# Kernel tuning notes

Measured on AMD Instinct MI355X. Metric: run time of the kernel, lower is better.

## Reference

```python
import jax, jax.numpy as jnp
import numpy as np

B, H, W, D = 4, 64, 64, 384
M, P = 12, 9
DH = D // M             # 32 head dim
DFF = 3 * D             # 1152 FFN hidden
N = H * W               # 4096 queries (single level)


def setup_inputs():
    key = jax.random.key(0)
    ks = jax.random.split(key, 12)
    g = lambda k, s, sc=0.02: jax.random.normal(k, s, jnp.float32) * sc
    return {
        "x": jax.random.normal(ks[0], (B, D, H, W), jnp.float32),
        "qry_masks": jnp.zeros((B, H, W), jnp.float32),
        "so_w": g(ks[1], (M * P * 2, D)), "so_b": g(ks[2], (M * P * 2,)),
        "aw_w": g(ks[3], (M * P, D)), "aw_b": g(ks[4], (M * P,)),
        "vp_w": g(ks[5], (D, D)), "vp_b": jnp.zeros((D,), jnp.float32),
        "op_w": g(ks[6], (D, D)), "op_b": jnp.zeros((D,), jnp.float32),
        "ln1_g": jnp.ones((D,), jnp.float32), "ln1_b": jnp.zeros((D,), jnp.float32),
        "w1": g(ks[7], (DFF, D)), "w2": g(ks[8], (D, DFF)),
        "ln2_g": jnp.ones((D,), jnp.float32), "ln2_b": jnp.zeros((D,), jnp.float32),
        "level_embed": g(ks[9], (1, D), 1.0),
    }


def _layernorm(x, g, b, eps=1e-5):
    mu = x.mean(-1, keepdims=True)
    v = ((x - mu) ** 2).mean(-1, keepdims=True)
    return (x - mu) * jax.lax.rsqrt(v + eps) * g + b


def _sine_pos(mask):
    # mask: [B,H,W] bool. mmdet SinePositionalEncoding(num_feats=D//2, normalize=True)
    not_mask = (~mask).astype(jnp.float32)
    y = jnp.cumsum(not_mask, 1)
    x = jnp.cumsum(not_mask, 2)
    eps, scale = 1e-6, 2.0 * np.pi
    y = y / (y[:, -1:, :] + eps) * scale
    x = x / (x[:, :, -1:] + eps) * scale
    nf = D // 2
    dim_t = 10000.0 ** (2.0 * (jnp.arange(nf) // 2).astype(jnp.float32) / nf)
    px, py = x[..., None] / dim_t, y[..., None] / dim_t

    def interleave(p):
        return jnp.stack([jnp.sin(p[..., 0::2]), jnp.cos(p[..., 1::2])], -1).reshape(p.shape[:-1] + (nf,))

    return jnp.concatenate([interleave(py), interleave(px)], -1)  # [B,H,W,D]


def _bilinear_gather(v, px, py):
    # v: [B,M,HW,DH]; px,py: [B,M,NP] pixel coords (grid_sample align_corners=False, zero pad)
    x0 = jnp.floor(px); y0 = jnp.floor(py)
    lx, ly = px - x0, py - y0
    x0i, y0i = x0.astype(jnp.int32), y0.astype(jnp.int32)
    out = jnp.zeros(v.shape[:2] + (px.shape[-1], v.shape[-1]), v.dtype)
    for dx, dy, wgt in ((0, 0, (1 - lx) * (1 - ly)), (1, 0, lx * (1 - ly)),
                        (0, 1, (1 - lx) * ly), (1, 1, lx * ly)):
        xi, yi = x0i + dx, y0i + dy
        valid = ((xi >= 0) & (xi < W) & (yi >= 0) & (yi < H)).astype(v.dtype)
        idx = jnp.clip(yi, 0, H - 1) * W + jnp.clip(xi, 0, W - 1)
        g = jnp.take_along_axis(v, idx[..., None], axis=2)  # [B,M,NP,DH]
        out = out + (wgt * valid)[..., None] * g
    return out


def _msdeform_attn(q, value_in, ref, mask_flat,
                   so_w, so_b, aw_w, aw_b, vp_w, vp_b, op_w, op_b):
    value = value_in @ vp_w.T + vp_b                      # [B,N,D]
    value = jnp.where(mask_flat[..., None], 0.0, value)
    so = (q @ so_w.T + so_b).reshape(B, N, M, P, 2)       # single level
    aw = jax.nn.softmax((q @ aw_w.T + aw_b).reshape(B, N, M, P), axis=-1)
    norm = jnp.array([W, H], jnp.float32)
    loc = ref[:, :, None, None, :] + so / norm            # [B,N,M,P,2] in [0,1]
    v = value.reshape(B, N, M, DH).transpose(0, 2, 1, 3)  # [B,M,HW,DH]
    px = (loc[..., 0] * W - 0.5).transpose(0, 2, 1, 3).reshape(B, M, N * P)
    py = (loc[..., 1] * H - 0.5).transpose(0, 2, 1, 3).reshape(B, M, N * P)
    sampled = _bilinear_gather(v, px, py).reshape(B, M, N, P, DH)
    out = jnp.einsum('bmnpd,bnmp->bnmd', sampled, aw).reshape(B, N, D)
    return out @ op_w.T + op_b


def reference(x, qry_masks, so_w, so_b, aw_w, aw_b, vp_w, vp_b, op_w, op_b,
              ln1_g, ln1_b, w1, w2, ln2_g, ln2_b, level_embed):
    mask = (qry_masks == 255.0)                           # [B,H,W] bool
    pos = _sine_pos(mask).reshape(B, N, D) + level_embed[0]
    src = x.reshape(B, D, N).transpose(0, 2, 1)           # [B,N,D]
    mask_flat = mask.reshape(B, N)
    gy, gx = jnp.meshgrid((jnp.arange(H, dtype=jnp.float32) + 0.5) / H,
                          (jnp.arange(W, dtype=jnp.float32) + 0.5) / W, indexing='ij')
    ref = jnp.stack([gx.reshape(-1), gy.reshape(-1)], -1)[None]  # [1,N,2] (x,y)
    q = src
    attn = _msdeform_attn(q + pos, q, ref, mask_flat,
                          so_w, so_b, aw_w, aw_b, vp_w, vp_b, op_w, op_b)
    q = _layernorm(q + attn, ln1_g, ln1_b)
    q = _layernorm(q + jax.nn.relu(q @ w1.T) @ w2.T, ln2_g, ln2_b)
    return q.transpose(0, 2, 1).reshape(B, D, H, W)
```

## Files before the change

### kernel.cpp

```cpp
#include <hip/hip_runtime.h>
#include <math.h>

#define Bc   4
#define Hc   64
#define Wc   64
#define Dc   384
#define Nc   4096
#define Mc   12
#define Pc   9
#define DHc  32
#define DFFc 1152
#define BNc  (Bc*Nc)

typedef __attribute__((ext_vector_type(8))) short short8;
typedef __attribute__((ext_vector_type(4))) float floatx4;

__device__ __forceinline__ ushort f2bf(float f) {
    union { float f; unsigned u; } v; v.f = f;
    unsigned r = v.u + 0x7fffu + ((v.u >> 16) & 1u);
    return (ushort)(r >> 16);
}
__device__ __forceinline__ float bf2f(ushort u) {
    union { unsigned u; float f; } v; v.u = (unsigned)u << 16; return v.f;
}

__device__ __forceinline__ void gload_lds16(const void* g, void* l) {
    __builtin_amdgcn_global_load_lds(
        (const __attribute__((address_space(1))) void*)(uintptr_t)g,
        (__attribute__((address_space(3))) void*)(uintptr_t)l,
        16, 0, 0);
}

#define SOW_N  82944
#define AWW_N  41472
#define VPW_N  147456
#define OPW_N  147456
#define W1_N   442368
#define W2_N   442368
#define WTOT   1304064

__global__ void init_kernel(const float* __restrict__ so_w,
                            const float* __restrict__ aw_w,
                            const float* __restrict__ vp_w,
                            const float* __restrict__ op_w,
                            const float* __restrict__ w1,
                            const float* __restrict__ w2,
                            const float* __restrict__ so_b,
                            const float* __restrict__ aw_b,
                            const float* __restrict__ qmask,
                            ushort* __restrict__ out,
                            float* __restrict__ bias_out,
                            float* __restrict__ cum_y,
                            float* __restrict__ cum_x) {
    int i = blockIdx.x * 256 + threadIdx.x;
    if (i < WTOT) {
        float v;
        int j = i;
        if (j < SOW_N) v = so_w[j];
        else if ((j -= SOW_N) < AWW_N) v = aw_w[j];
        else if ((j -= AWW_N) < VPW_N) v = vp_w[j];
        else if ((j -= VPW_N) < OPW_N) v = op_w[j];
        else if ((j -= OPW_N) < W1_N)  v = w1[j];
        else { j -= W1_N; v = w2[j]; }
        out[i] = f2bf(v);
        return;
    }
    int j = i - WTOT;
    if (j < 384) {
        bias_out[j] = (j < 216) ? so_b[j] : (j < 324 ? aw_b[j - 216] : 0.f);
        return;
    }
    int t = j - 384;
    if (t < Bc * Wc) {
        int b = t / Wc, w = t % Wc;
        float run = 0.f;
        for (int h = 0; h < Hc; ++h) {
            run += (qmask[(b * Hc + h) * Wc + w] == 255.0f) ? 0.f : 1.f;
            cum_y[(b * Hc + h) * Wc + w] = run;
        }
    } else if (t < Bc * Wc + Bc * Hc) {
        int t2 = t - Bc * Wc;
        int b = t2 / Hc, h = t2 % Hc;
        float run = 0.f;
        for (int w = 0; w < Wc; ++w) {
            run += (qmask[(b * Hc + h) * Wc + w] == 255.0f) ? 0.f : 1.f;
            cum_x[(b * Hc + h) * Wc + w] = run;
        }
    }
}

__global__ void transpose_pos_kernel(const float* __restrict__ x,
                                     const float* __restrict__ cum_y,
                                     const float* __restrict__ cum_x,
                                     const float* __restrict__ level_embed,
                                     ushort* __restrict__ src_bf,
                                     ushort* __restrict__ qpos_bf) {
    __shared__ float tile[32][33];
    int b  = blockIdx.z;
    int n0 = blockIdx.x * 32, d0 = blockIdx.y * 32;
    int tx = threadIdx.x, ty = threadIdx.y;
    tile[ty][tx] = x[((size_t)b * Dc + (d0 + ty)) * Nc + (n0 + tx)];
    __syncthreads();
    int n = n0 + ty, d = d0 + tx;
    float v = tile[tx][ty];
    size_t oi = ((size_t)b * Nc + n) * Dc + d;
    src_bf[oi] = f2bf(v);
    int h = n >> 6, w = n & 63;
    const float TWO_PI = 6.28318530717958647692f;
    float vy = cum_y[(b * Hc + h) * Wc + w] /
               (cum_y[(b * Hc + (Hc - 1)) * Wc + w] + 1e-6f) * TWO_PI;
    float vx = cum_x[(b * Hc + h) * Wc + w] /
               (cum_x[(b * Hc + h) * Wc + (Wc - 1)] + 1e-6f) * TWO_PI;
    int   i  = (d < 192) ? d : d - 192;
    float vv = (d < 192) ? vy : vx;
    float e   = (float)(i >> 1) * (2.0f / 192.0f);
    float idt = exp2f(e * -13.28771237954945f);
    float ang = vv * idt;
    float pe  = (i & 1) ? __cosf(ang) : __sinf(ang);
    qpos_bf[oi] = f2bf(v + pe + level_embed[d]);
}

template <int KT>
__device__ __forceinline__ void gemm_core(
        const ushort* __restrict__ A, const ushort* __restrict__ Wt,
        const float* __restrict__ bias,
        float* __restrict__ Cf, ushort* __restrict__ Cb,
        int Nout, int relu, const float* __restrict__ qmask,
        ushort* As, ushort* Bs) {
    constexpr int NCH = KT / 32;
    const int tid  = threadIdx.x;
    const int m0   = blockIdx.x * 128;
    const int n0   = blockIdx.y * 128;
    const int lane = tid & 63;
    const int wv   = tid >> 6;
    const int wr   = (wv >> 1) * 64;
    const int wc   = (wv & 1) * 64;
    const int quad = lane >> 4;
    const int lrow = lane & 15;
    const int srow = wv * 32 + (lane >> 2);
    const int scol = (lane & 3) * 8;

    floatx4 acc[4][4];
    #pragma unroll
    for (int i = 0; i < 4; ++i)
        #pragma unroll
        for (int j = 0; j < 4; ++j)
            acc[i][j] = (floatx4)(0.f);

    #pragma unroll
    for (int s = 0; s < 2; ++s) {
        gload_lds16(A  + (size_t)(m0 + srow + s * 16) * KT + scol,
                    As + wv * 1024 + s * 512);
        gload_lds16(Wt + (size_t)(n0 + srow + s * 16) * KT + scol,
                    Bs + wv * 1024 + s * 512);
    }

    for (int c = 0; c < NCH; ++c) {
        const int cur = c & 1;
        __syncthreads();
        if (c + 1 < NCH) {
            const int k0 = (c + 1) * 32;
            #pragma unroll
            for (int s = 0; s < 2; ++s) {
                gload_lds16(A  + (size_t)(m0 + srow + s * 16) * KT + k0 + scol,
                            As + (cur ^ 1) * 4096 + wv * 1024 + s * 512);
                gload_lds16(Wt + (size_t)(n0 + srow + s * 16) * KT + k0 + scol,
                            Bs + (cur ^ 1) * 4096 + wv * 1024 + s * 512);
            }
        }
        short8 afr[4], bfr[4];
        #pragma unroll
        for (int i = 0; i < 4; ++i)
            afr[i] = *(const short8*)(As + cur * 4096 +
                                      (wr + i * 16 + lrow) * 32 + quad * 8);
        #pragma unroll
        for (int j = 0; j < 4; ++j)
            bfr[j] = *(const short8*)(Bs + cur * 4096 +
                                      (wc + j * 16 + lrow) * 32 + quad * 8);
        #pragma unroll
        for (int i = 0; i < 4; ++i)
            #pragma unroll
            for (int j = 0; j < 4; ++j)
                acc[i][j] = __builtin_amdgcn_mfma_f32_16x16x32_bf16(
                    afr[i], bfr[j], acc[i][j], 0, 0, 0);
    }

    float mz[4][4];
    #pragma unroll
    for (int i = 0; i < 4; ++i)
        #pragma unroll
        for (int r = 0; r < 4; ++r) {
            int row = m0 + wr + i * 16 + quad * 4 + r;
            mz[i][r] = (qmask && qmask[row] == 255.0f) ? 0.f : 1.f;
        }

    #pragma unroll
    for (int i = 0; i < 4; ++i) {
        #pragma unroll
        for (int j = 0; j < 4; ++j) {
            int col = n0 + wc + j * 16 + lrow;
            if (col >= Nout) continue;
            float bsv = bias ? bias[col] : 0.f;
            #pragma unroll
            for (int r = 0; r < 4; ++r) {
                int row = m0 + wr + i * 16 + quad * 4 + r;
                float v = acc[i][j][r] + bsv;
                if (relu) v = fmaxf(v, 0.f);
                v *= mz[i][r];
                if (Cf) Cf[(size_t)row * Nout + col] = v;
                if (Cb) Cb[(size_t)row * Nout + col] = f2bf(v);
            }
        }
    }
}

template <int KT>
__global__ __launch_bounds__(256) void gemm_single_kernel(
        const ushort* __restrict__ A, const ushort* __restrict__ Wt,
        const float* __restrict__ bias,
        float* __restrict__ Cf, ushort* __restrict__ Cb,
        int Nout, int relu, const float* __restrict__ qmask) {
    __shared__ ushort As[2 * 128 * 32];
    __shared__ ushort Bs[2 * 128 * 32];
    gemm_core<KT>(A, Wt, bias, Cf, Cb, Nout, relu, qmask, As, Bs);
}

__global__ __launch_bounds__(256) void gemm_dual_kernel(
        const ushort* __restrict__ A0, const ushort* __restrict__ W0,
        const float* __restrict__ b0, float* __restrict__ Cf0,
        const ushort* __restrict__ A1, const ushort* __restrict__ W1,
        const float* __restrict__ b1, ushort* __restrict__ Cb1,
        const float* __restrict__ qmask) {
    __shared__ ushort As[2 * 128 * 32];
    __shared__ ushort Bs[2 * 128 * 32];
    if (blockIdx.z == 0)
        gemm_core<384>(A0, W0, b0, Cf0, nullptr, 384, 0, nullptr, As, Bs);
    else
        gemm_core<384>(A1, W1, b1, nullptr, Cb1, 384, 0, qmask, As, Bs);
}

template <int KT, int MODE>
__global__ __launch_bounds__(512) void gemm_fullrow_kernel(
        const ushort* __restrict__ A, const ushort* __restrict__ Wt,
        const float* __restrict__ bias, const void* __restrict__ resid,
        const float* __restrict__ g, const float* __restrict__ beta,
        float* __restrict__ outf, ushort* __restrict__ outb) {
    constexpr int NCH = KT / 32;
    __shared__ ushort smem[28672];
    __shared__ float eps1[8][64], eps2[8][64];
    __shared__ float mu_l[64], rs_l[64];
    ushort* As = smem;
    ushort* Bs = smem + 4096;
    const int tid  = threadIdx.x;
    const int lane = tid & 63;
    const int wv   = tid >> 6;
    const int quad = lane >> 4;
    const int lrow = lane & 15;
    const int m0   = blockIdx.x * 64;
    const int srow = lane >> 2;
    const int scol = (lane & 3) * 8;

    floatx4 acc[4][3];
    #pragma unroll
    for (int i = 0; i < 4; ++i)
        #pragma unroll
        for (int j = 0; j < 3; ++j)
            acc[i][j] = (floatx4)(0.f);

    if (wv < 4)
        gload_lds16(A + (size_t)(m0 + wv * 16 + srow) * KT + scol,
                    As + wv * 512);
    #pragma unroll
    for (int s = 0; s < 3; ++s)
        gload_lds16(Wt + (size_t)(wv * 48 + s * 16 + srow) * KT + scol,
                    Bs + wv * 1536 + s * 512);

    for (int c = 0; c < NCH; ++c) {
        const int cur = c & 1;
        __syncthreads();
        if (c + 1 < NCH) {
            const int k0 = (c + 1) * 32;
            if (wv < 4)
                gload_lds16(A + (size_t)(m0 + wv * 16 + srow) * KT + k0 + scol,
                            As + (cur ^ 1) * 2048 + wv * 512);
            #pragma unroll
            for (int s = 0; s < 3; ++s)
                gload_lds16(Wt + (size_t)(wv * 48 + s * 16 + srow) * KT + k0 + scol,
                            Bs + (cur ^ 1) * 12288 + wv * 1536 + s * 512);
        }
        short8 afr[4], bfr[3];
        #pragma unroll
        for (int i = 0; i < 4; ++i)
            afr[i] = *(const short8*)(As + cur * 2048 +
                                      (i * 16 + lrow) * 32 + quad * 8);
        #pragma unroll
        for (int j = 0; j < 3; ++j)
            bfr[j] = *(const short8*)(Bs + cur * 12288 +
                                      (wv * 48 + j * 16 + lrow) * 32 + quad * 8);
        #pragma unroll
        for (int i = 0; i < 4; ++i)
            #pragma unroll
            for (int j = 0; j < 3; ++j)
                acc[i][j] = __builtin_amdgcn_mfma_f32_16x16x32_bf16(
                    afr[i], bfr[j], acc[i][j], 0, 0, 0);
    }

    float s1[16], s2[16];
    #pragma unroll
    for (int k = 0; k < 16; ++k) { s1[k] = 0.f; s2[k] = 0.f; }
    #pragma unroll
    for (int i = 0; i < 4; ++i) {
        #pragma unroll
        for (int r = 0; r < 4; ++r) {
            int rl = i * 16 + quad * 4 + r;
            #pragma unroll
            for (int j = 0; j < 3; ++j) {
                int col = wv * 48 + j * 16 + lrow;
                float t = acc[i][j][r];
                if (bias) t += bias[col];
                if (MODE == 0)
                    t += bf2f(((const ushort*)resid)[(size_t)(m0 + rl) * Dc + col]);
                else
                    t += ((const float*)resid)[(size_t)(m0 + rl) * Dc + col];
                acc[i][j][r] = t;
                s1[i * 4 + r] += t;
                s2[i * 4 + r] += t * t;
            }
        }
    }
    #pragma unroll
    for (int m = 1; m < 16; m <<= 1) {
        #pragma unroll
        for (int k = 0; k < 16; ++k) {
            s1[k] += __shfl_xor(s1[k], m);
            s2[k] += __shfl_xor(s2[k], m);
        }
    }
    if (lrow == 0) {
        #pragma unroll
        for (int i = 0; i < 4; ++i)
            #pragma unroll
            for (int r = 0; r < 4; ++r) {
                int rl = i * 16 + quad * 4 + r;
                eps1[wv][rl] = s1[i * 4 + r];
                eps2[wv][rl] = s2[i * 4 + r];
            }
    }
    __syncthreads();
    if (tid < 64) {
        float a1 = 0.f, a2 = 0.f;
        #pragma unroll
        for (int w = 0; w < 8; ++w) { a1 += eps1[w][tid]; a2 += eps2[w][tid]; }
        float mu  = a1 * (1.0f / Dc);
        float var = a2 * (1.0f / Dc) - mu * mu;
        mu_l[tid] = mu;
        rs_l[tid] = rsqrtf(var + 1e-5f);
    }
    __syncthreads();

    #pragma unroll
    for (int i = 0; i < 4; ++i) {
        #pragma unroll
        for (int r = 0; r < 4; ++r) {
            int rl = i * 16 + quad * 4 + r;
            float mu = mu_l[rl], rs = rs_l[rl];
            #pragma unroll
            for (int j = 0; j < 3; ++j) {
                int col = wv * 48 + j * 16 + lrow;
                acc[i][j][r] = (acc[i][j][r] - mu) * rs * g[col] + beta[col];
            }
        }
    }

    if (MODE == 0) {
        #pragma unroll
        for (int i = 0; i < 4; ++i)
            #pragma unroll
            for (int j = 0; j < 3; ++j) {
                int col = wv * 48 + j * 16 + lrow;
                #pragma unroll
                for (int r = 0; r < 4; ++r) {
                    int rl = i * 16 + quad * 4 + r;
                    float v = acc[i][j][r];
                    outf[(size_t)(m0 + rl) * Dc + col] = v;
                    outb[(size_t)(m0 + rl) * Dc + col] = f2bf(v);
                }
            }
    } else {
        float* tile = (float*)smem;
        const int b   = m0 >> 12;
        const int n0r = m0 & 4095;
        #pragma unroll
        for (int gp = 0; gp < 2; ++gp) {
            __syncthreads();
            if ((wv >> 2) == gp) {
                int cbase = (wv & 3) * 48;
                #pragma unroll
                for (int i = 0; i < 4; ++i)
                    #pragma unroll
                    for (int j = 0; j < 3; ++j) {
                        int c = cbase + j * 16 + lrow;
                        #pragma unroll
                        for (int r = 0; r < 4; ++r) {
                            int rl = i * 16 + quad * 4 + r;
                            tile[rl * 193 + c] = acc[i][j][r];
                        }
                    }
            }
            __syncthreads();
            const int row = tid & 63;
            const int cp  = tid >> 6;
            #pragma unroll
            for (int it = 0; it < 24; ++it) {
                int c = it * 8 + cp;
                outf[((size_t)(b * Dc + gp * 192 + c)) * Nc + n0r + row] =
                    tile[row * 193 + c];
            }
        }
    }
}

__global__ __launch_bounds__(256) void deform_attn_kernel(
        const ushort* __restrict__ value_bf, const float* __restrict__ soaw,
        ushort* __restrict__ out) {
    int bid = blockIdx.x;
    int gb  = (bid & 7) * 384 + (bid >> 3);
    int gid = gb * 64 + (threadIdx.x >> 2);
    int l4  = threadIdx.x & 3;
    int m  = gid % Mc;
    int bn = gid / Mc;
    int b  = bn >> 12;
    int n  = bn & 4095;
    int h  = n >> 6, w = n & 63;
    const float* sop = soaw + (size_t)bn * 384 + m * 18;
    const float* lgt = soaw + (size_t)bn * 384 + 216 + m * Pc;
    float awv[Pc];
    float mx = lgt[0];
    #pragma unroll
    for (int i = 1; i < Pc; ++i) mx = fmaxf(mx, lgt[i]);
    float ssum = 0.f;
    #pragma unroll
    for (int i = 0; i < Pc; ++i) { awv[i] = __expf(lgt[i] - mx); ssum += awv[i]; }
    float sinv = 1.f / ssum;
    const ushort* vb = value_bf + ((size_t)b * Nc) * Dc + m * DHc + l4 * 8;
    float acc[8] = {0.f, 0.f, 0.f, 0.f, 0.f, 0.f, 0.f, 0.f};
    #pragma unroll
    for (int p = 0; p < Pc; ++p) {
        float2 so2 = *(const float2*)(sop + p * 2);
        float px = (float)w + so2.x;
        float py = (float)h + so2.y;
        float x0f = floorf(px), y0f = floorf(py);
        float lx = px - x0f, ly = py - y0f;
        int x0 = (int)x0f, y0 = (int)y0f;
        int x1 = x0 + 1,  y1 = y0 + 1;
        float a = awv[p] * sinv;
        float w00 = (1.f - lx) * (1.f - ly) * a;
        float w01 = lx * (1.f - ly) * a;
        float w10 = (1.f - lx) * ly * a;
        float w11 = lx * ly * a;
        bool bx0 = (unsigned)x0 < 64u, bx1 = (unsigned)x1 < 64u;
        bool by0 = (unsigned)y0 < 64u, by1 = (unsigned)y1 < 64u;
        w00 = (bx0 && by0) ? w00 : 0.f;
        w01 = (bx1 && by0) ? w01 : 0.f;
        w10 = (bx0 && by1) ? w10 : 0.f;
        w11 = (bx1 && by1) ? w11 : 0.f;
        int cx0 = min(max(x0, 0), 63), cx1 = min(max(x1, 0), 63);
        int cy0 = min(max(y0, 0), 63), cy1 = min(max(y1, 0), 63);
        uint4 q00 = *(const uint4*)(vb + (size_t)(cy0 * 64 + cx0) * Dc);
        uint4 q01 = *(const uint4*)(vb + (size_t)(cy0 * 64 + cx1) * Dc);
        uint4 q10 = *(const uint4*)(vb + (size_t)(cy1 * 64 + cx0) * Dc);
        uint4 q11 = *(const uint4*)(vb + (size_t)(cy1 * 64 + cx1) * Dc);
        union { unsigned u; float f; } t;
        #define ACC2(word, wg, k)                                   \
            t.u = (word) << 16;         acc[k]     += (wg) * t.f;   \
            t.u = (word) & 0xffff0000u; acc[k + 1] += (wg) * t.f;
        #define ACC8(q, wg) \
            ACC2((q).x, wg, 0) ACC2((q).y, wg, 2) ACC2((q).z, wg, 4) ACC2((q).w, wg, 6)
        ACC8(q00, w00) ACC8(q01, w01) ACC8(q10, w10) ACC8(q11, w11)
        #undef ACC8
        #undef ACC2
    }
    short8 o;
    #pragma unroll
    for (int k = 0; k < 8; ++k) o[k] = (short)f2bf(acc[k]);
    *(short8*)(out + (size_t)bn * Dc + m * DHc + l4 * 8) = o;
}

extern "C" void kernel_launch(void* const* d_in, const int* in_sizes, int n_in,
                              void* d_out, int out_size, void* d_ws, size_t ws_size,
                              hipStream_t stream) {
    (void)in_sizes; (void)n_in; (void)out_size; (void)ws_size;
    const float* x      = (const float*)d_in[0];
    const float* qmask  = (const float*)d_in[1];
    const float* so_w   = (const float*)d_in[2];
    const float* so_b   = (const float*)d_in[3];
    const float* aw_w   = (const float*)d_in[4];
    const float* aw_b   = (const float*)d_in[5];
    const float* vp_w   = (const float*)d_in[6];
    const float* vp_b   = (const float*)d_in[7];
    const float* op_w   = (const float*)d_in[8];
    const float* op_b   = (const float*)d_in[9];
    const float* ln1_g  = (const float*)d_in[10];
    const float* ln1_b  = (const float*)d_in[11];
    const float* w1     = (const float*)d_in[12];
    const float* w2     = (const float*)d_in[13];
    const float* ln2_g  = (const float*)d_in[14];
    const float* ln2_b  = (const float*)d_in[15];
    const float* lvl    = (const float*)d_in[16];
    float* out = (float*)d_out;

    float*  ws       = (float*)d_ws;
    float*  q1_f     = ws;
    ushort* src_bf   = (ushort*)(q1_f + 6291456);
    ushort* qpos_bf  = src_bf + 6291456;
    ushort* value_bf = qpos_bf + 6291456;
    ushort* hbuf_bf  = value_bf + 6291456;
    float*  soaw_f   = (float*)hbuf_bf;
    ushort* wbuf     = hbuf_bf + 18874368;
    float*  soaw_bias= (float*)(wbuf + 1304064);
    float*  cum_y    = soaw_bias + 384;
    float*  cum_x    = cum_y + 16384;

    const ushort* soaw_wb = wbuf;
    const ushort* vp_wb = soaw_wb + SOW_N + AWW_N;
    const ushort* op_wb = vp_wb + VPW_N;
    const ushort* w1_b  = op_wb + OPW_N;
    const ushort* w2_b  = w1_b + W1_N;

    init_kernel<<<(WTOT + 384 + 512 + 255) / 256, 256, 0, stream>>>(
        so_w, aw_w, vp_w, op_w, w1, w2, so_b, aw_b, qmask,
        wbuf, soaw_bias, cum_y, cum_x);
    transpose_pos_kernel<<<dim3(Nc / 32, Dc / 32, Bc), dim3(32, 32), 0, stream>>>(
        x, cum_y, cum_x, lvl, src_bf, qpos_bf);
    gemm_dual_kernel<<<dim3(BNc / 128, 3, 2), 256, 0, stream>>>(
        qpos_bf, soaw_wb, soaw_bias, soaw_f,
        src_bf, vp_wb, vp_b, value_bf, qmask);
    deform_attn_kernel<<<(BNc * Mc) / 64, 256, 0, stream>>>(
        value_bf, soaw_f, qpos_bf);
    gemm_fullrow_kernel<384, 0><<<BNc / 64, 512, 0, stream>>>(
        qpos_bf, op_wb, op_b, src_bf, ln1_g, ln1_b, q1_f, qpos_bf);
    gemm_single_kernel<384><<<dim3(BNc / 128, 9), 256, 0, stream>>>(
        qpos_bf, w1_b, nullptr, nullptr, hbuf_bf, DFFc, 1, nullptr);
    gemm_fullrow_kernel<1152, 1><<<BNc / 64, 512, 0, stream>>>(
        hbuf_bf, w2_b, nullptr, q1_f, ln2_g, ln2_b, out, nullptr);
}
```

Before: 265.0 us.

## Pipeline fullrow GEMM with per-wave weight buffers and regroup deform-attn blocks

```diff
diff --git a/kernel.cpp b/kernel.cpp
--- a/kernel.cpp
+++ b/kernel.cpp
@@ -240,17 +240,15 @@
 }
 
 template <int KT, int MODE>
-__global__ __launch_bounds__(512) void gemm_fullrow_kernel(
+__global__ __launch_bounds__(512, 2) void gemm_fullrow_kernel(
         const ushort* __restrict__ A, const ushort* __restrict__ Wt,
         const float* __restrict__ bias, const void* __restrict__ resid,
         const float* __restrict__ g, const float* __restrict__ beta,
         float* __restrict__ outf, ushort* __restrict__ outb) {
     constexpr int NCH = KT / 32;
-    __shared__ ushort smem[28672];
+    __shared__ ushort Bs[8 * 3 * 1536];
     __shared__ float eps1[8][64], eps2[8][64];
     __shared__ float mu_l[64], rs_l[64];
-    ushort* As = smem;
-    ushort* Bs = smem + 4096;
     const int tid  = threadIdx.x;
     const int lane = tid & 63;
     const int wv   = tid >> 6;
@@ -260,6 +258,10 @@
     const int srow = lane >> 2;
     const int scol = (lane & 3) * 8;
 
+    ushort* BsW = Bs + wv * (3 * 1536);
+    const ushort* wsrc  = Wt + (size_t)(wv * 48 + srow) * KT + scol;
+    const ushort* abase = A  + (size_t)(m0 + lrow) * KT + quad * 8;
+
     floatx4 acc[4][3];
     #pragma unroll
     for (int i = 0; i < 4; ++i)
@@ -267,43 +269,48 @@
         for (int j = 0; j < 3; ++j)
             acc[i][j] = (floatx4)(0.f);
 
-    if (wv < 4)
-        gload_lds16(A + (size_t)(m0 + wv * 16 + srow) * KT + scol,
-                    As + wv * 512);
-    #pragma unroll
-    for (int s = 0; s < 3; ++s)
-        gload_lds16(Wt + (size_t)(wv * 48 + s * 16 + srow) * KT + scol,
-                    Bs + wv * 1536 + s * 512);
-
-    for (int c = 0; c < NCH; ++c) {
-        const int cur = c & 1;
-        __syncthreads();
-        if (c + 1 < NCH) {
-            const int k0 = (c + 1) * 32;
-            if (wv < 4)
-                gload_lds16(A + (size_t)(m0 + wv * 16 + srow) * KT + k0 + scol,
-                            As + (cur ^ 1) * 2048 + wv * 512);
-            #pragma unroll
-            for (int s = 0; s < 3; ++s)
-                gload_lds16(Wt + (size_t)(wv * 48 + s * 16 + srow) * KT + k0 + scol,
-                            Bs + (cur ^ 1) * 12288 + wv * 1536 + s * 512);
-        }
-        short8 afr[4], bfr[3];
-        #pragma unroll
-        for (int i = 0; i < 4; ++i)
-            afr[i] = *(const short8*)(As + cur * 2048 +
-                                      (i * 16 + lrow) * 32 + quad * 8);
-        #pragma unroll
-        for (int j = 0; j < 3; ++j)
-            bfr[j] = *(const short8*)(Bs + cur * 12288 +
-                                      (wv * 48 + j * 16 + lrow) * 32 + quad * 8);
-        #pragma unroll
-        for (int i = 0; i < 4; ++i)
-            #pragma unroll
-            for (int j = 0; j < 3; ++j)
-                acc[i][j] = __builtin_amdgcn_mfma_f32_16x16x32_bf16(
-                    afr[i], bfr[j], acc[i][j], 0, 0, 0);
-    }
+#define STAGE_W(c, buf)                                                      \
+    gload_lds16(wsrc + (size_t)0 * 16 * KT + (c) * 32, BsW + (buf) * 1536);  \
+    gload_lds16(wsrc + (size_t)1 * 16 * KT + (c) * 32, BsW + (buf) * 1536 + 512); \
+    gload_lds16(wsrc + (size_t)2 * 16 * KT + (c) * 32, BsW + (buf) * 1536 + 1024);
+
+#define LOAD_A(dst, c)                                                       \
+    dst[0] = *(const short8*)(abase + (size_t)0 * 16 * KT + (c) * 32);       \
+    dst[1] = *(const short8*)(abase + (size_t)1 * 16 * KT + (c) * 32);       \
+    dst[2] = *(const short8*)(abase + (size_t)2 * 16 * KT + (c) * 32);       \
+    dst[3] = *(const short8*)(abase + (size_t)3 * 16 * KT + (c) * 32);
+
+#define DO_MFMA(afr, buf)                                                    \
+    {   short8 bfr[3];                                                       \
+        bfr[0] = *(const short8*)(BsW + (buf) * 1536 + (lrow)      * 32 + quad * 8); \
+        bfr[1] = *(const short8*)(BsW + (buf) * 1536 + (16 + lrow) * 32 + quad * 8); \
+        bfr[2] = *(const short8*)(BsW + (buf) * 1536 + (32 + lrow) * 32 + quad * 8); \
+        _Pragma("unroll")                                                    \
+        for (int i_ = 0; i_ < 4; ++i_) {                                     \
+            acc[i_][0] = __builtin_amdgcn_mfma_f32_16x16x32_bf16(afr[i_], bfr[0], acc[i_][0], 0, 0, 0); \
+            acc[i_][1] = __builtin_amdgcn_mfma_f32_16x16x32_bf16(afr[i_], bfr[1], acc[i_][1], 0, 0, 0); \
+            acc[i_][2] = __builtin_amdgcn_mfma_f32_16x16x32_bf16(afr[i_], bfr[2], acc[i_][2], 0, 0, 0); \
+        } }
+
+    short8 afrC[4], afrN[4];
+    LOAD_A(afrC, 0)
+    STAGE_W(0, 0)
+    STAGE_W(1, 1)
+
+    for (int c = 0; c < NCH - 1; ++c) {
+        asm volatile("s_waitcnt vmcnt(3)" ::: "memory");
+        LOAD_A(afrN, c + 1)
+        if (c + 2 < NCH) { STAGE_W(c + 2, (c + 2) % 3) }
+        DO_MFMA(afrC, c % 3)
+        #pragma unroll
+        for (int i = 0; i < 4; ++i) afrC[i] = afrN[i];
+    }
+    asm volatile("s_waitcnt vmcnt(0)" ::: "memory");
+    DO_MFMA(afrC, (NCH - 1) % 3)
+
+#undef STAGE_W
+#undef LOAD_A
+#undef DO_MFMA
 
     float s1[16], s2[16];
     #pragma unroll
@@ -329,11 +336,11 @@
         }
     }
     #pragma unroll
-    for (int m = 1; m < 16; m <<= 1) {
+    for (int mm = 1; mm < 16; mm <<= 1) {
         #pragma unroll
         for (int k = 0; k < 16; ++k) {
-            s1[k] += __shfl_xor(s1[k], m);
-            s2[k] += __shfl_xor(s2[k], m);
+            s1[k] += __shfl_xor(s1[k], mm);
+            s2[k] += __shfl_xor(s2[k], mm);
         }
     }
     if (lrow == 0) {
@@ -387,7 +394,7 @@
                 }
             }
     } else {
-        float* tile = (float*)smem;
+        float* tile = (float*)Bs;
         const int b   = m0 >> 12;
         const int n0r = m0 & 4095;
         #pragma unroll
@@ -423,15 +430,15 @@
 __global__ __launch_bounds__(256) void deform_attn_kernel(
         const ushort* __restrict__ value_bf, const float* __restrict__ soaw,
         ushort* __restrict__ out) {
-    int bid = blockIdx.x;
-    int gb  = (bid & 7) * 384 + (bid >> 3);
-    int gid = gb * 64 + (threadIdx.x >> 2);
-    int l4  = threadIdx.x & 3;
-    int m  = gid % Mc;
-    int bn = gid / Mc;
-    int b  = bn >> 12;
-    int n  = bn & 4095;
-    int h  = n >> 6, w = n & 63;
+    int bid   = blockIdx.x;
+    int slice = bid % 48;
+    int h     = bid / 48;
+    int m  = slice % Mc;
+    int b  = slice / Mc;
+    int w  = threadIdx.x >> 2;
+    int l4 = threadIdx.x & 3;
+    int n  = (h << 6) | w;
+    int bn = b * Nc + n;
     const float* sop = soaw + (size_t)bn * 384 + m * 18;
     const float* lgt = soaw + (size_t)bn * 384 + 216 + m * Pc;
     float awv[Pc];
@@ -535,7 +542,7 @@
     gemm_dual_kernel<<<dim3(BNc / 128, 3, 2), 256, 0, stream>>>(
         qpos_bf, soaw_wb, soaw_bias, soaw_f,
         src_bf, vp_wb, vp_b, value_bf, qmask);
-    deform_attn_kernel<<<(BNc * Mc) / 64, 256, 0, stream>>>(
+    deform_attn_kernel<<<3072, 256, 0, stream>>>(
         value_bf, soaw_f, qpos_bf);
     gemm_fullrow_kernel<384, 0><<<BNc / 64, 512, 0, stream>>>(
         qpos_bf, op_wb, op_b, src_bf, ln1_g, ln1_b, q1_f, qpos_bf);
```

Measured after the change: 292.9 us. +10.5%, slower.
